# Optimization experiments

Hardware: AMD Instinct MI355X
Metric: run time of the kernel (lower is better)

The kernel has to match this reference:

```python
import jax, jax.numpy as jnp
import numpy as np

N_NODES = 50000
N_EDGES = 400000
N_GRAPHS = 256
D = 200
N_STEPS = 6


def setup_inputs() -> dict:
    key = jax.random.key(0)
    ks = jax.random.split(key, 10)
    s = 1.0 / np.sqrt(D)
    x = jax.random.normal(ks[0], (N_NODES, D), dtype=jnp.float32)
    edge_index = jax.random.randint(ks[1], (2, N_EDGES), 0, N_NODES, dtype=jnp.int64)
    batch = jnp.sort(jax.random.randint(ks[2], (N_NODES,), 0, N_GRAPHS, dtype=jnp.int64))
    ggnn_weight = jax.random.uniform(ks[3], (N_STEPS, D, D), jnp.float32, -s, s)
    w_ih = jax.random.uniform(ks[4], (3 * D, D), jnp.float32, -s, s)
    w_hh = jax.random.uniform(ks[5], (3 * D, D), jnp.float32, -s, s)
    b_ih = jax.random.uniform(ks[6], (3 * D,), jnp.float32, -s, s)
    b_hh = jax.random.uniform(ks[7], (3 * D,), jnp.float32, -s, s)
    cls_w = jax.random.uniform(ks[8], (2, D), jnp.float32, -s, s)
    cls_b = jax.random.uniform(ks[9], (2,), jnp.float32, -s, s)
    return {"x": x, "edge_index": edge_index, "batch": batch,
            "ggnn_weight": ggnn_weight, "w_ih": w_ih, "w_hh": w_hh,
            "b_ih": b_ih, "b_hh": b_hh, "cls_w": cls_w, "cls_b": cls_b}


def _gru_cell(m, h, w_ih, w_hh, b_ih, b_hh):
    gi = m @ w_ih.T + b_ih            # [N, 3D]
    gh = h @ w_hh.T + b_hh            # [N, 3D]
    i_r, i_z, i_n = jnp.split(gi, 3, axis=-1)
    h_r, h_z, h_n = jnp.split(gh, 3, axis=-1)
    r = jax.nn.sigmoid(i_r + h_r)
    z = jax.nn.sigmoid(i_z + h_z)
    n = jnp.tanh(i_n + r * h_n)
    return (1.0 - z) * n + z * h


def reference(x, edge_index, batch, ggnn_weight, w_ih, w_hh, b_ih, b_hh, cls_w, cls_b):
    src, dst = edge_index[0], edge_index[1]

    def step(h, W):
        m = h @ W                                        # [N, D]
        agg = jax.ops.segment_sum(m[src], dst, num_segments=N_NODES)  # scatter-add
        return _gru_cell(agg, h, w_ih, w_hh, b_ih, b_hh), None

    h, _ = jax.lax.scan(step, x, ggnn_weight)
    h = jax.nn.relu(h)
    pooled = jax.ops.segment_max(h, batch, num_segments=N_GRAPHS)    # [G, D]
    logits = pooled @ cls_w.T + cls_b                                # [G, 2]
    return jax.nn.sigmoid(logits)
```

## Files before the change

kernel.cpp:

```cpp
#include <hip/hip_runtime.h>
#include <cstdint>
#include <cstddef>

#define NN 50000
#define NE 400000
#define NG 256
#define DIM 200
#define NSTEPS 6

typedef unsigned int uint;
typedef unsigned short ushort;
typedef __attribute__((ext_vector_type(8))) short short8;
typedef __attribute__((ext_vector_type(4))) float f32x4;

#define GLL16(gsrc, ldst)                                                        \
  __builtin_amdgcn_global_load_lds(                                              \
      (const __attribute__((address_space(1))) void*)(gsrc),                     \
      (__attribute__((address_space(3))) void*)(ldst), 16, 0, 0)

__device__ __forceinline__ float bfu(ushort u) { return __uint_as_float((uint)u << 16); }
__device__ __forceinline__ uint packf(float v) {
  uint u = __float_as_uint(v);
  uint t = u + 0x7fffu + ((u >> 16) & 1u);
  uint hb = t & 0xffff0000u;
  float lo = v - __uint_as_float(hb);
  uint ul = __float_as_uint(lo);
  uint t2 = ul + 0x7fffu + ((ul >> 16) & 1u);
  return hb | (t2 >> 16);
}
__device__ __forceinline__ uint packf_tr(float v) {
  uint u = __float_as_uint(v);
  uint t = u + 0x7fffu + ((u >> 16) & 1u);
  uint hb = t & 0xffff0000u;
  float lo = v - __uint_as_float(hb);
  return hb | (__float_as_uint(lo) >> 16);
}
__device__ __forceinline__ ushort bf16rn(float v) {
  uint u = __float_as_uint(v);
  return (ushort)((u + 0x7fffu + ((u >> 16) & 1u)) >> 16);
}
__device__ __forceinline__ float fsig(float x) {
  return __builtin_amdgcn_rcpf(1.f + __expf(-x));
}
__device__ __forceinline__ float ftanh(float x) {
  return 1.f - 2.f * __builtin_amdgcn_rcpf(__expf(2.f * x) + 1.f);
}

__global__ void k_zero_i32(int* __restrict__ p, int n) {
  for (int i = blockIdx.x * blockDim.x + threadIdx.x; i < n; i += gridDim.x * blockDim.x)
    p[i] = 0;
}
__global__ void k_zero_f32(float* __restrict__ p, int n) {
  for (int i = blockIdx.x * blockDim.x + threadIdx.x; i < n; i += gridDim.x * blockDim.x)
    p[i] = 0.f;
}
__global__ void k_hist(const int* __restrict__ dst, int* __restrict__ cnt, int nE) {
  int e = blockIdx.x * blockDim.x + threadIdx.x;
  if (e < nE) atomicAdd(&cnt[dst[e]], 1);
}

__global__ __launch_bounds__(256) void k_scan_blk(const int* __restrict__ cnt,
                                                  int* __restrict__ incl,
                                                  int* __restrict__ bsum, int n) {
  __shared__ int buf[256];
  int i = blockIdx.x * 256 + threadIdx.x;
  int v = (i < n) ? cnt[i] : 0;
  buf[threadIdx.x] = v;
  __syncthreads();
#pragma unroll
  for (int d = 1; d < 256; d <<= 1) {
    int t = (threadIdx.x >= d) ? buf[threadIdx.x - d] : 0;
    __syncthreads();
    buf[threadIdx.x] += t;
    __syncthreads();
  }
  if (i < n) incl[i] = buf[threadIdx.x];
  if (threadIdx.x == 255) bsum[blockIdx.x] = buf[255];
}
__global__ __launch_bounds__(256) void k_scan_top(int* __restrict__ bsum, int nb) {
  __shared__ int buf[256];
  int v = (threadIdx.x < nb) ? bsum[threadIdx.x] : 0;
  buf[threadIdx.x] = v;
  __syncthreads();
#pragma unroll
  for (int d = 1; d < 256; d <<= 1) {
    int t = (threadIdx.x >= d) ? buf[threadIdx.x - d] : 0;
    __syncthreads();
    buf[threadIdx.x] += t;
    __syncthreads();
  }
  if (threadIdx.x < nb) bsum[threadIdx.x] = buf[threadIdx.x] - v;
}
__global__ __launch_bounds__(256) void k_scan_fin(const int* __restrict__ cnt,
                                                  const int* __restrict__ incl,
                                                  const int* __restrict__ bsum,
                                                  int* __restrict__ off,
                                                  int* __restrict__ cursor, int n) {
  int i = blockIdx.x * 256 + threadIdx.x;
  if (i < n) {
    int o = incl[i] + bsum[blockIdx.x];
    off[i + 1] = o;
    cursor[i] = o - cnt[i];
  }
  if (i == 0) off[0] = 0;
}

__global__ void k_scatter(const int* __restrict__ dst, const int* __restrict__ src,
                          int* __restrict__ cursor, int* __restrict__ slist, int nE) {
  int e = blockIdx.x * blockDim.x + threadIdx.x;
  if (e < nE) {
    int d = dst[e];
    int pos = atomicAdd(&cursor[d], 1);
    slist[pos] = src[e];
  }
}

__global__ void k_pack_split(const float* __restrict__ x, ushort* __restrict__ hHi,
                             ushort* __restrict__ hLo, int n8) {
  for (int i = blockIdx.x * blockDim.x + threadIdx.x; i < n8;
       i += gridDim.x * blockDim.x) {
    const float* s = x + (size_t)i * 8;
    uint hi[4], lo[4];
#pragma unroll
    for (int j = 0; j < 4; ++j) {
      uint w0 = packf(s[j * 2]), w1 = packf(s[j * 2 + 1]);
      hi[j] = (w0 >> 16) | (w1 & 0xffff0000u);
      lo[j] = (w0 & 0xffffu) | (w1 << 16);
    }
    *reinterpret_cast<uint4*>(hHi + (size_t)i * 8) = make_uint4(hi[0], hi[1], hi[2], hi[3]);
    *reinterpret_cast<uint4*>(hLo + (size_t)i * 8) = make_uint4(lo[0], lo[1], lo[2], lo[3]);
  }
}

__global__ void k_pack_bf(const float* __restrict__ in, ushort* __restrict__ out, int n) {
  for (int i = blockIdx.x * blockDim.x + threadIdx.x; i < n; i += gridDim.x * blockDim.x)
    out[i] = bf16rn(in[i]);
}

#define GBM 64
#define GBN 64
#define GBK 8
__global__ __launch_bounds__(256) void k_gemm_wc(const float* __restrict__ gg,
                                                 const float* __restrict__ w_ih,
                                                 ushort* __restrict__ wcB) {
  __shared__ __align__(16) float As[GBK][GBM];
  __shared__ __align__(16) float Bs[GBK][GBN];
  int s = blockIdx.z;
  const float* A = gg + (size_t)s * DIM * DIM;
  ushort* out = wcB + (size_t)s * 3 * DIM * DIM;
  int tid = threadIdx.x;
  int row0 = blockIdx.y * GBM;
  int col0 = blockIdx.x * GBN;
  int ty = tid >> 4, tx = tid & 15;
  float acc[4][4] = {};
  for (int k0 = 0; k0 < DIM; k0 += GBK) {
    {
      int r = tid >> 2;
      int kk = (tid & 3) * 2;
      int gr = row0 + r;
      float2 v = make_float2(0.f, 0.f);
      if (gr < DIM) v = *reinterpret_cast<const float2*>(&A[(size_t)gr * DIM + k0 + kk]);
      As[kk][r] = v.x; As[kk + 1][r] = v.y;
    }
    {
      int n = tid >> 2;
      int kk = (tid & 3) * 2;
      int gn = col0 + n;
      float2 v = *reinterpret_cast<const float2*>(&w_ih[(size_t)gn * DIM + k0 + kk]);
      Bs[kk][n] = v.x; Bs[kk + 1][n] = v.y;
    }
    __syncthreads();
#pragma unroll
    for (int k = 0; k < GBK; ++k) {
      float4 av = *reinterpret_cast<const float4*>(&As[k][ty * 4]);
      float4 bv = *reinterpret_cast<const float4*>(&Bs[k][tx * 4]);
      float a[4] = {av.x, av.y, av.z, av.w};
      float b[4] = {bv.x, bv.y, bv.z, bv.w};
#pragma unroll
      for (int i = 0; i < 4; ++i)
#pragma unroll
        for (int j = 0; j < 4; ++j) acc[i][j] += a[i] * b[j];
    }
    __syncthreads();
  }
#pragma unroll
  for (int i = 0; i < 4; ++i) {
    int r = row0 + ty * 4 + i;
    if (r >= DIM) continue;
#pragma unroll
    for (int j = 0; j < 4; ++j) {
      int c = col0 + tx * 4 + j;
      out[(size_t)c * DIM + r] = bf16rn(acc[i][j]);
    }
  }
}

__global__ __launch_bounds__(256) void k_aggregate_hi(const ushort* __restrict__ hHi,
                                                      const int* __restrict__ off,
                                                      const int* __restrict__ slist,
                                                      ushort* __restrict__ aggHi) {
  int wid = blockIdx.x * 4 + (threadIdx.x >> 6);
  int half = (threadIdx.x >> 5) & 1;
  int node = wid * 2 + half;
  int lane32 = threadIdx.x & 31;
  bool nok = node < NN;
  bool act = (lane32 < 25) && nok;
  const uint4* hb = reinterpret_cast<const uint4*>(hHi);
  float a[8] = {};
  int beg = 0, end = 0;
  if (nok) { beg = off[node]; end = off[node + 1]; }
  int p = beg;
#define ACC8(q)                                                   \
  {                                                               \
    a[0] += __uint_as_float((q).x << 16);                         \
    a[1] += __uint_as_float((q).x & 0xffff0000u);                 \
    a[2] += __uint_as_float((q).y << 16);                         \
    a[3] += __uint_as_float((q).y & 0xffff0000u);                 \
    a[4] += __uint_as_float((q).z << 16);                         \
    a[5] += __uint_as_float((q).z & 0xffff0000u);                 \
    a[6] += __uint_as_float((q).w << 16);                         \
    a[7] += __uint_as_float((q).w & 0xffff0000u);                 \
  }
  for (; p + 3 < end; p += 4) {
    int s0 = slist[p], s1 = slist[p + 1], s2 = slist[p + 2], s3 = slist[p + 3];
    if (act) {
      uint4 q0 = hb[(size_t)s0 * 25 + lane32];
      uint4 q1 = hb[(size_t)s1 * 25 + lane32];
      uint4 q2 = hb[(size_t)s2 * 25 + lane32];
      uint4 q3 = hb[(size_t)s3 * 25 + lane32];
      ACC8(q0) ACC8(q1) ACC8(q2) ACC8(q3)
    }
  }
  for (; p < end; ++p) {
    int s = slist[p];
    if (act) {
      uint4 q = hb[(size_t)s * 25 + lane32];
      ACC8(q)
    }
  }
#undef ACC8
  if (act) {
    uint w[4];
#pragma unroll
    for (int j = 0; j < 4; ++j)
      w[j] = (uint)bf16rn(a[j * 2]) | ((uint)bf16rn(a[j * 2 + 1]) << 16);
    reinterpret_cast<uint4*>(aggHi)[(size_t)node * 25 + lane32] =
        make_uint4(w[0], w[1], w[2], w[3]);
  }
}

#define NPAN 391
#define PPC 3
#define NCHK 131
#define NCOLB 7
#define GRIDF 917

#define MFMA16(a, b, c) __builtin_amdgcn_mfma_f32_16x16x32_bf16(a, b, c, 0, 0, 0)

__global__ __launch_bounds__(256, 2) void k_fused_mfma(
    const ushort* __restrict__ aggHi, const ushort* __restrict__ hHi,
    const ushort* __restrict__ hLo,
    const ushort* __restrict__ wcB, const ushort* __restrict__ whB,
    const float* __restrict__ b_ih, const float* __restrict__ b_hh,
    ushort* __restrict__ hnHi, ushort* __restrict__ hnLo) {
  __shared__ uint4 Bb[6][25][32];

  int tid = threadIdx.x;
  int lane = tid & 63;
  int wv = tid >> 6;
  int lr = lane & 15;
  int kc = lane >> 4;

  int x = blockIdx.x & 7, ii = blockIdx.x >> 3;
  int work = (x < 5 ? x * 115 : 575 + (x - 5) * 114) + ii;
  int chunk = work / NCOLB;
  int col = work - chunk * NCOLB;
  int cc0 = col * 32;

  {
    uint4* BbF = &Bb[0][0][0];
    for (int i2 = 0; i2 < 19; ++i2) {
      int u = tid + i2 * 256;
      if (u < 4800) {
        int mat = u / 800;
        int rem = u - mat * 800;
        int ch = rem >> 5;
        int c = rem & 31;
        int gc = cc0 + c; if (gc > 199) gc = 199;
        const ushort* wsrc = (mat & 1) ? whB : wcB;
        GLL16(wsrc + (size_t)((mat >> 1) * DIM + gc) * DIM + ch * 8, BbF + u);
      }
    }
  }
  __syncthreads();

  for (int j = 0; j < PPC; ++j) {
    int p = chunk * PPC + j;
    if (p >= NPAN) break;
    int prow0 = p * 128;
    int r0 = prow0 + wv * 32 + lr;
    int r1 = r0 + 16;
    int rc0 = r0 < NN ? r0 : NN - 1;
    int rc1 = r1 < NN ? r1 : NN - 1;
    const ushort* a0 = aggHi + (size_t)rc0 * DIM;
    const ushort* a1 = aggHi + (size_t)rc1 * DIM;
    const ushort* h0 = hHi + (size_t)rc0 * DIM;
    const ushort* h1 = hHi + (size_t)rc1 * DIM;

    f32x4 acc[3][2][2][2] = {};
    short8 aq[4][2][2];
    ushort hvh[2][2][4], hvl[2][2][4];

#define LDA(d, t)                                                              \
  {                                                                            \
    const bool v_ = ((t) < 6) || (kc == 0);                                    \
    const int of_ = v_ ? ((t) * 32 + kc * 8) : 0;                              \
    const short8 z_ = {0, 0, 0, 0, 0, 0, 0, 0};                                \
    aq[d][0][0] = v_ ? *reinterpret_cast<const short8*>(a0 + of_) : z_;        \
    aq[d][0][1] = v_ ? *reinterpret_cast<const short8*>(a1 + of_) : z_;        \
    aq[d][1][0] = v_ ? *reinterpret_cast<const short8*>(h0 + of_) : z_;        \
    aq[d][1][1] = v_ ? *reinterpret_cast<const short8*>(h1 + of_) : z_;        \
  }

    LDA(0, 0)
    LDA(1, 1)
    LDA(2, 2)
#pragma unroll
    for (int t = 0; t < 7; ++t) {
      const int cur = t & 3;
      if (t < 4) LDA((t + 3) & 3, t + 3)
      if (t == 5) {
#pragma unroll
        for (int ct = 0; ct < 2; ++ct) {
          int c = cc0 + ct * 16 + lr; if (c > 199) c = 199;
#pragma unroll
          for (int rf = 0; rf < 2; ++rf) {
#pragma unroll
            for (int qq = 0; qq < 4; ++qq) {
              int r_ = prow0 + wv * 32 + rf * 16 + kc * 4 + qq;
              int rc = r_ < NN ? r_ : NN - 1;
              size_t base = (size_t)rc * DIM + c;
              hvh[ct][rf][qq] = hHi[base];
              hvl[ct][rf][qq] = hLo[base];
            }
          }
        }
      }
      int bch = t * 4 + kc; if (bch > 24) bch = 24;
#pragma unroll
      for (int g = 0; g < 3; ++g) {
#pragma unroll
        for (int ct = 0; ct < 2; ++ct) {
          short8 b1 = *reinterpret_cast<const short8*>(&Bb[g * 2 + 0][bch][ct * 16 + lr]);
          short8 b2 = *reinterpret_cast<const short8*>(&Bb[g * 2 + 1][bch][ct * 16 + lr]);
#pragma unroll
          for (int rf = 0; rf < 2; ++rf) {
            acc[g][0][rf][ct] = MFMA16(aq[cur][0][rf], b1, acc[g][0][rf][ct]);
            acc[g][1][rf][ct] = MFMA16(aq[cur][1][rf], b2, acc[g][1][rf][ct]);
          }
        }
      }
    }
#undef LDA

#pragma unroll
    for (int ct = 0; ct < 2; ++ct) {
      int c = cc0 + ct * 16 + lr;
      if (c >= DIM) continue;
      float bir = b_ih[c], biz = b_ih[DIM + c], bin = b_ih[2 * DIM + c];
      float bhr = b_hh[c], bhz = b_hh[DIM + c], bhn = b_hh[2 * DIM + c];
#pragma unroll
      for (int rf = 0; rf < 2; ++rf) {
#pragma unroll
        for (int qq = 0; qq < 4; ++qq) {
          int r_ = prow0 + wv * 32 + rf * 16 + kc * 4 + qq;
          if (r_ >= NN) continue;
          size_t base = (size_t)r_ * DIM + c;
          float gir = acc[0][0][rf][ct][qq] + bir;
          float giz = acc[1][0][rf][ct][qq] + biz;
          float gin = acc[2][0][rf][ct][qq] + bin;
          float ghr = acc[0][1][rf][ct][qq] + bhr;
          float ghz = acc[1][1][rf][ct][qq] + bhz;
          float ghn = acc[2][1][rf][ct][qq] + bhn;
          float rr = fsig(gir + ghr);
          float zz = fsig(giz + ghz);
          float nn = ftanh(gin + rr * ghn);
          float hv = bfu(hvh[ct][rf][qq]) + bfu(hvl[ct][rf][qq]);
          uint w = packf_tr((1.f - zz) * nn + zz * hv);
          hnHi[base] = (ushort)(w >> 16);
          hnLo[base] = (ushort)(w & 0xffffu);
        }
      }
    }
  }
}

__global__ __launch_bounds__(256) void k_pool(const ushort* __restrict__ hHi,
                                              const ushort* __restrict__ hLo,
                                              const int* __restrict__ batch,
                                              float* __restrict__ pooled) {
  int i = blockIdx.x;
  int j = threadIdx.x;
  if (j < DIM) {
    int g = batch[i];
    size_t base = (size_t)i * DIM + j;
    float v = bfu(hHi[base]) + bfu(hLo[base]);
    v = v > 0.f ? v : 0.f;
    atomicMax((int*)&pooled[(size_t)g * DIM + j], __float_as_int(v));
  }
}

__global__ __launch_bounds__(256) void k_classify(const float* __restrict__ pooled,
                                                  const float* __restrict__ w,
                                                  const float* __restrict__ b,
                                                  float* __restrict__ out) {
  __shared__ float r0[256], r1[256];
  int g = blockIdx.x;
  int j = threadIdx.x;
  float p = (j < DIM) ? pooled[(size_t)g * DIM + j] : 0.f;
  r0[j] = (j < DIM) ? p * w[j] : 0.f;
  r1[j] = (j < DIM) ? p * w[DIM + j] : 0.f;
  __syncthreads();
  for (int d = 128; d > 0; d >>= 1) {
    if (j < d) { r0[j] += r0[j + d]; r1[j] += r1[j + d]; }
    __syncthreads();
  }
  if (j == 0) {
    out[g * 2 + 0] = 1.f / (1.f + expf(-(r0[0] + b[0])));
    out[g * 2 + 1] = 1.f / (1.f + expf(-(r1[0] + b[1])));
  }
}

extern "C" void kernel_launch(void* const* d_in, const int* in_sizes, int n_in,
                              void* d_out, int out_size, void* d_ws, size_t ws_size,
                              hipStream_t stream) {
  const float* x = (const float*)d_in[0];
  const int* edge_index = (const int*)d_in[1];
  const int* batch = (const int*)d_in[2];
  const float* ggnn_w = (const float*)d_in[3];
  const float* w_ih = (const float*)d_in[4];
  const float* w_hh = (const float*)d_in[5];
  const float* b_ih = (const float*)d_in[6];
  const float* b_hh = (const float*)d_in[7];
  const float* cls_w = (const float*)d_in[8];
  const float* cls_b = (const float*)d_in[9];
  float* out = (float*)d_out;

  const int* src = edge_index;
  const int* dst = edge_index + NE;

  char* wsb = (char*)d_ws;
  size_t off = 0;
  auto alloc = [&](size_t bytes) -> void* {
    void* p = wsb + off;
    off += (bytes + 255) & ~(size_t)255;
    return p;
  };
  ushort* hHiA = (ushort*)alloc((size_t)NN * DIM * 2);
  ushort* hLoA = (ushort*)alloc((size_t)NN * DIM * 2);
  ushort* hHiB = (ushort*)alloc((size_t)NN * DIM * 2);
  ushort* hLoB = (ushort*)alloc((size_t)NN * DIM * 2);
  ushort* aggHi = (ushort*)alloc((size_t)NN * DIM * 2);
  ushort* wcB = (ushort*)alloc((size_t)NSTEPS * 3 * DIM * DIM * 2);
  ushort* whB = (ushort*)alloc((size_t)3 * DIM * DIM * 2);
  float* pooled = (float*)alloc((size_t)NG * DIM * 4);
  int* indeg = (int*)alloc((size_t)NN * 4);
  int* offs = (int*)alloc((size_t)(NN + 1) * 4);
  int* incl = (int*)alloc((size_t)NN * 4);
  int* bsum = (int*)alloc((size_t)256 * 4);
  int* cursor = (int*)alloc((size_t)NN * 4);
  int* slist = (int*)alloc((size_t)NE * 4);
  if (off > ws_size) return;

  const int NB = (NN + 255) / 256;

  k_pack_split<<<2048, 256, 0, stream>>>(x, hHiA, hLoA, NN * DIM / 8);

  k_zero_i32<<<196, 256, 0, stream>>>(indeg, NN);
  k_hist<<<(NE + 255) / 256, 256, 0, stream>>>(dst, indeg, NE);
  k_scan_blk<<<NB, 256, 0, stream>>>(indeg, incl, bsum, NN);
  k_scan_top<<<1, 256, 0, stream>>>(bsum, NB);
  k_scan_fin<<<NB, 256, 0, stream>>>(indeg, incl, bsum, offs, cursor, NN);
  k_scatter<<<(NE + 255) / 256, 256, 0, stream>>>(dst, src, cursor, slist, NE);

  {
    dim3 g((3 * DIM + GBN - 1) / GBN, (DIM + GBM - 1) / GBM, NSTEPS);
    k_gemm_wc<<<g, 256, 0, stream>>>(ggnn_w, w_ih, wcB);
    k_pack_bf<<<512, 256, 0, stream>>>(w_hh, whB, 3 * DIM * DIM);
  }

  ushort* hHic = hHiA;
  ushort* hLoc = hLoA;
  ushort* hHin = hHiB;
  ushort* hLon = hLoB;
  for (int s = 0; s < NSTEPS; ++s) {
    k_aggregate_hi<<<(NN / 2 + 3) / 4, 256, 0, stream>>>(hHic, offs, slist, aggHi);
    k_fused_mfma<<<GRIDF, 256, 0, stream>>>(aggHi, hHic, hLoc,
                                            wcB + (size_t)s * 3 * DIM * DIM,
                                            whB, b_ih, b_hh, hHin, hLon);
    ushort* t;
    t = hHic; hHic = hHin; hHin = t;
    t = hLoc; hLoc = hLon; hLon = t;
  }

  k_zero_f32<<<200, 256, 0, stream>>>(pooled, NG * DIM);
  k_pool<<<NN, 256, 0, stream>>>(hHic, hLoc, batch, pooled);
  k_classify<<<NG, 256, 0, stream>>>(pooled, cls_w, cls_b, out);
}
```

Before: 669.9 us.

## Unroll gather loop by eight, hoist GRU biases and row indices, raise MFMA priority

The gather kernel gains an 8-way unrolled loop, so more independent row loads are in flight per node. The GRU kernel loads its biases once per block instead of per panel, precomputes row offsets as 32-bit values, and wraps the MFMA block in s_setprio so matrix work is favoured across waves. The final blend becomes a single fma. These are several small independent tweaks, and together they raise register pressure.

```diff
diff --git a/kernel.cpp b/kernel.cpp
--- a/kernel.cpp
+++ b/kernel.cpp
@@ -221,14 +221,22 @@
     a[6] += __uint_as_float((q).w << 16);                         \
     a[7] += __uint_as_float((q).w & 0xffff0000u);                 \
   }
+  for (; p + 7 < end; p += 8) {
+    uint4 q[8];
+    if (act) {
+#pragma unroll
+      for (int e = 0; e < 8; ++e) q[e] = hb[(size_t)slist[p + e] * 25 + lane32];
+#pragma unroll
+      for (int e = 0; e < 8; ++e) ACC8(q[e])
+    }
+  }
   for (; p + 3 < end; p += 4) {
-    int s0 = slist[p], s1 = slist[p + 1], s2 = slist[p + 2], s3 = slist[p + 3];
+    uint4 q[4];
     if (act) {
-      uint4 q0 = hb[(size_t)s0 * 25 + lane32];
-      uint4 q1 = hb[(size_t)s1 * 25 + lane32];
-      uint4 q2 = hb[(size_t)s2 * 25 + lane32];
-      uint4 q3 = hb[(size_t)s3 * 25 + lane32];
-      ACC8(q0) ACC8(q1) ACC8(q2) ACC8(q3)
+#pragma unroll
+      for (int e = 0; e < 4; ++e) q[e] = hb[(size_t)slist[p + e] * 25 + lane32];
+#pragma unroll
+      for (int e = 0; e < 4; ++e) ACC8(q[e])
     }
   }
   for (; p < end; ++p) {
@@ -276,6 +284,21 @@
   int chunk = work / NCOLB;
   int col = work - chunk * NCOLB;
   int cc0 = col * 32;
+
+  int c0 = cc0 + lr;
+  int c1 = c0 + 16;
+  bool c0ok = c0 < DIM, c1ok = c1 < DIM;
+  int c0c = c0ok ? c0 : DIM - 1;
+  int c1c = c1ok ? c1 : DIM - 1;
+
+  float bias[2][6];
+#pragma unroll
+  for (int ct = 0; ct < 2; ++ct) {
+    int c = ct ? c1c : c0c;
+    bias[ct][0] = b_ih[c];           bias[ct][1] = b_ih[DIM + c];
+    bias[ct][2] = b_ih[2 * DIM + c]; bias[ct][3] = b_hh[c];
+    bias[ct][4] = b_hh[DIM + c];     bias[ct][5] = b_hh[2 * DIM + c];
+  }
 
   {
     uint4* BbF = &Bb[0][0][0];
@@ -307,6 +330,17 @@
     const ushort* h0 = hHi + (size_t)rc0 * DIM;
     const ushort* h1 = hHi + (size_t)rc1 * DIM;
 
+    uint rbase[2][4];
+    bool rok[2][4];
+#pragma unroll
+    for (int rf = 0; rf < 2; ++rf)
+#pragma unroll
+      for (int qq = 0; qq < 4; ++qq) {
+        int r_ = prow0 + wv * 32 + rf * 16 + kc * 4 + qq;
+        rok[rf][qq] = r_ < NN;
+        rbase[rf][qq] = (uint)(r_ < NN ? r_ : NN - 1) * DIM;
+      }
+
     f32x4 acc[3][2][2][2] = {};
     short8 aq[4][2][2];
     ushort hvh[2][2][4], hvl[2][2][4];
@@ -332,21 +366,19 @@
       if (t == 5) {
 #pragma unroll
         for (int ct = 0; ct < 2; ++ct) {
-          int c = cc0 + ct * 16 + lr; if (c > 199) c = 199;
-#pragma unroll
-          for (int rf = 0; rf < 2; ++rf) {
+          int cc = ct ? c1c : c0c;
+#pragma unroll
+          for (int rf = 0; rf < 2; ++rf)
 #pragma unroll
             for (int qq = 0; qq < 4; ++qq) {
-              int r_ = prow0 + wv * 32 + rf * 16 + kc * 4 + qq;
-              int rc = r_ < NN ? r_ : NN - 1;
-              size_t base = (size_t)rc * DIM + c;
+              uint base = rbase[rf][qq] + cc;
               hvh[ct][rf][qq] = hHi[base];
               hvl[ct][rf][qq] = hLo[base];
             }
-          }
         }
       }
       int bch = t * 4 + kc; if (bch > 24) bch = 24;
+      __builtin_amdgcn_s_setprio(1);
 #pragma unroll
       for (int g = 0; g < 3; ++g) {
 #pragma unroll
@@ -360,33 +392,31 @@
           }
         }
       }
+      __builtin_amdgcn_s_setprio(0);
     }
 #undef LDA
 
 #pragma unroll
     for (int ct = 0; ct < 2; ++ct) {
-      int c = cc0 + ct * 16 + lr;
-      if (c >= DIM) continue;
-      float bir = b_ih[c], biz = b_ih[DIM + c], bin = b_ih[2 * DIM + c];
-      float bhr = b_hh[c], bhz = b_hh[DIM + c], bhn = b_hh[2 * DIM + c];
+      if (!(ct ? c1ok : c0ok)) continue;
+      int cc = ct ? c1 : c0;
 #pragma unroll
       for (int rf = 0; rf < 2; ++rf) {
 #pragma unroll
         for (int qq = 0; qq < 4; ++qq) {
-          int r_ = prow0 + wv * 32 + rf * 16 + kc * 4 + qq;
-          if (r_ >= NN) continue;
-          size_t base = (size_t)r_ * DIM + c;
-          float gir = acc[0][0][rf][ct][qq] + bir;
-          float giz = acc[1][0][rf][ct][qq] + biz;
-          float gin = acc[2][0][rf][ct][qq] + bin;
-          float ghr = acc[0][1][rf][ct][qq] + bhr;
-          float ghz = acc[1][1][rf][ct][qq] + bhz;
-          float ghn = acc[2][1][rf][ct][qq] + bhn;
+          if (!rok[rf][qq]) continue;
+          uint base = rbase[rf][qq] + cc;
+          float gir = acc[0][0][rf][ct][qq] + bias[ct][0];
+          float giz = acc[1][0][rf][ct][qq] + bias[ct][1];
+          float gin = acc[2][0][rf][ct][qq] + bias[ct][2];
+          float ghr = acc[0][1][rf][ct][qq] + bias[ct][3];
+          float ghz = acc[1][1][rf][ct][qq] + bias[ct][4];
+          float ghn = acc[2][1][rf][ct][qq] + bias[ct][5];
           float rr = fsig(gir + ghr);
           float zz = fsig(giz + ghz);
           float nn = ftanh(gin + rr * ghn);
           float hv = bfu(hvh[ct][rf][qq]) + bfu(hvl[ct][rf][qq]);
-          uint w = packf_tr((1.f - zz) * nn + zz * hv);
+          uint w = packf_tr(fmaf(zz, hv - nn, nn));
           hnHi[base] = (ushort)(w >> 16);
           hnLo[base] = (ushort)(w & 0xffffu);
         }
```

After: 640.4 us. 4.4% less time.
